# Performance work log

Hardware: AMD Instinct MI355X
Metric: run time of the kernel (lower is better)

The kernel has to match this reference:

```python
import math
import jax, jax.numpy as jnp
import numpy as np

N_TOKENS = 16384
IN_FEATURES = 4096
N_EXPERTS = 64
TOP_K = 2
CAPACITY_FACTOR = 1.25
# get_capacity(n_tokens * top_k, n_experts, capacity_factor)
CAPACITY = math.ceil(N_TOKENS * TOP_K / N_EXPERTS * CAPACITY_FACTOR)  # 640


def setup_inputs() -> dict:
    key = jax.random.key(0)
    kx, kw = jax.random.split(key)
    x = jax.random.normal(kx, (N_TOKENS, IN_FEATURES), dtype=jnp.float32)
    W = jax.random.normal(kw, (N_EXPERTS, IN_FEATURES), dtype=jnp.float32) * (1.0 / math.sqrt(IN_FEATURES))
    return {"x": x, "W": W}


def reference(x, W):
    # gate: Linear(in_features, n_experts, bias=False)
    logits = jnp.einsum("nd,ed->ne", x, W)  # [N, E]
    n, e = logits.shape

    # pre_softmax=False path: topk over logits then softmax over the k scores
    scores, top_idx = jax.lax.top_k(logits, TOP_K)              # [N, K]
    probs = jax.nn.softmax(scores.astype(jnp.float32), axis=-1).astype(logits.dtype)

    rows = jnp.arange(n)[:, None]                               # [N, 1]
    # scatter probs / ones into dense [N, E] masks (topk indices per row are unique)
    top_k_masked_gates = jnp.zeros_like(logits).at[rows, top_idx].set(probs)
    top_k_mask = jnp.zeros_like(logits).at[rows, top_idx].set(1.0)

    # capacity top-k along the token dim (dim=0) -> per-expert token selection
    _, cap_idx = jax.lax.top_k(top_k_masked_gates.T, CAPACITY)  # [E, CAP] token ids
    cap_mask = jnp.zeros_like(logits).at[cap_idx, jnp.arange(e)[:, None]].set(1.0)

    # pad_to_capacity=False branch
    final_mask = jnp.logical_and(top_k_mask > 0, cap_mask > 0)  # [N, E]
    drop_mask = jnp.logical_not(final_mask)
    exceed_mask = jnp.take_along_axis(drop_mask, top_idx, axis=1)  # [N, K]
    final_probs = probs * jnp.logical_not(exceed_mask)
    final_indices = jnp.where(exceed_mask, jnp.iinfo(jnp.int32).max, top_idx)
    tokens_per_expert_before_capacity = top_k_mask.sum(0)       # [E]

    return final_probs, final_indices, tokens_per_expert_before_capacity
```

## Files before the change

kernel.cpp:

```cpp
#include <hip/hip_runtime.h>
#include <math.h>

#define N_TOK  16384
#define DIM    4096
#define NE     64
#define CAP    640
#define KC     32
#define TM     128
#define NTILES (N_TOK / TM)


__global__ __launch_bounds__(256) void gemm_logits_kernel(
    const float* __restrict__ x, const float* __restrict__ W,
    float* __restrict__ partials, int ks) {
  const int tile  = blockIdx.x % NTILES;
  const int split = blockIdx.x / NTILES;
  const int klen  = DIM / ks;
  const int k0    = split * klen;
  const int t_base = tile * TM;

  __shared__ float xT[2][KC][TM + 4];
  __shared__ float wT[2][KC][NE + 4];

  const int tid = threadIdx.x;
  const int lr = tid >> 3;
  const int lc = tid & 7;
  const int tg = tid >> 3;
  const int eg = tid & 7;

  float acc[4][8];
#pragma unroll
  for (int i = 0; i < 4; ++i)
#pragma unroll
    for (int j = 0; j < 8; ++j) acc[i][j] = 0.f;

  float4 rx0, rx1, rx2, rx3, rw0, rw1;

  {
    const int kg = k0;
    rx0 = *(const float4*)(x + (size_t)(t_base + lr +  0) * DIM + kg + lc * 4);
    rx1 = *(const float4*)(x + (size_t)(t_base + lr + 32) * DIM + kg + lc * 4);
    rx2 = *(const float4*)(x + (size_t)(t_base + lr + 64) * DIM + kg + lc * 4);
    rx3 = *(const float4*)(x + (size_t)(t_base + lr + 96) * DIM + kg + lc * 4);
    rw0 = *(const float4*)(W + (size_t)(lr +  0) * DIM + kg + lc * 4);
    rw1 = *(const float4*)(W + (size_t)(lr + 32) * DIM + kg + lc * 4);
    xT[0][lc * 4 + 0][lr +  0] = rx0.x; xT[0][lc * 4 + 1][lr +  0] = rx0.y;
    xT[0][lc * 4 + 2][lr +  0] = rx0.z; xT[0][lc * 4 + 3][lr +  0] = rx0.w;
    xT[0][lc * 4 + 0][lr + 32] = rx1.x; xT[0][lc * 4 + 1][lr + 32] = rx1.y;
    xT[0][lc * 4 + 2][lr + 32] = rx1.z; xT[0][lc * 4 + 3][lr + 32] = rx1.w;
    xT[0][lc * 4 + 0][lr + 64] = rx2.x; xT[0][lc * 4 + 1][lr + 64] = rx2.y;
    xT[0][lc * 4 + 2][lr + 64] = rx2.z; xT[0][lc * 4 + 3][lr + 64] = rx2.w;
    xT[0][lc * 4 + 0][lr + 96] = rx3.x; xT[0][lc * 4 + 1][lr + 96] = rx3.y;
    xT[0][lc * 4 + 2][lr + 96] = rx3.z; xT[0][lc * 4 + 3][lr + 96] = rx3.w;
    wT[0][lc * 4 + 0][lr +  0] = rw0.x; wT[0][lc * 4 + 1][lr +  0] = rw0.y;
    wT[0][lc * 4 + 2][lr +  0] = rw0.z; wT[0][lc * 4 + 3][lr +  0] = rw0.w;
    wT[0][lc * 4 + 0][lr + 32] = rw1.x; wT[0][lc * 4 + 1][lr + 32] = rw1.y;
    wT[0][lc * 4 + 2][lr + 32] = rw1.z; wT[0][lc * 4 + 3][lr + 32] = rw1.w;
  }

  const int niter = klen / KC;
  for (int it = 0; it < niter; ++it) {
    const int cur = it & 1;
    const int nxt = cur ^ 1;
    const bool more = (it + 1 < niter);

    if (more) {
      const int kg = k0 + (it + 1) * KC;
      rx0 = *(const float4*)(x + (size_t)(t_base + lr +  0) * DIM + kg + lc * 4);
      rx1 = *(const float4*)(x + (size_t)(t_base + lr + 32) * DIM + kg + lc * 4);
      rx2 = *(const float4*)(x + (size_t)(t_base + lr + 64) * DIM + kg + lc * 4);
      rx3 = *(const float4*)(x + (size_t)(t_base + lr + 96) * DIM + kg + lc * 4);
      rw0 = *(const float4*)(W + (size_t)(lr +  0) * DIM + kg + lc * 4);
      rw1 = *(const float4*)(W + (size_t)(lr + 32) * DIM + kg + lc * 4);
    }

    __syncthreads();

#pragma unroll
    for (int k = 0; k < KC; ++k) {
      const float4 xv = *(const float4*)&xT[cur][k][tg * 4];
      const float4 w0 = *(const float4*)&wT[cur][k][eg * 8];
      const float4 w1 = *(const float4*)&wT[cur][k][eg * 8 + 4];
      const float xa[4] = {xv.x, xv.y, xv.z, xv.w};
      const float wa[8] = {w0.x, w0.y, w0.z, w0.w, w1.x, w1.y, w1.z, w1.w};
#pragma unroll
      for (int i = 0; i < 4; ++i)
#pragma unroll
        for (int j = 0; j < 8; ++j)
          acc[i][j] = fmaf(xa[i], wa[j], acc[i][j]);
    }

    if (more) {
      xT[nxt][lc * 4 + 0][lr +  0] = rx0.x; xT[nxt][lc * 4 + 1][lr +  0] = rx0.y;
      xT[nxt][lc * 4 + 2][lr +  0] = rx0.z; xT[nxt][lc * 4 + 3][lr +  0] = rx0.w;
      xT[nxt][lc * 4 + 0][lr + 32] = rx1.x; xT[nxt][lc * 4 + 1][lr + 32] = rx1.y;
      xT[nxt][lc * 4 + 2][lr + 32] = rx1.z; xT[nxt][lc * 4 + 3][lr + 32] = rx1.w;
      xT[nxt][lc * 4 + 0][lr + 64] = rx2.x; xT[nxt][lc * 4 + 1][lr + 64] = rx2.y;
      xT[nxt][lc * 4 + 2][lr + 64] = rx2.z; xT[nxt][lc * 4 + 3][lr + 64] = rx2.w;
      xT[nxt][lc * 4 + 0][lr + 96] = rx3.x; xT[nxt][lc * 4 + 1][lr + 96] = rx3.y;
      xT[nxt][lc * 4 + 2][lr + 96] = rx3.z; xT[nxt][lc * 4 + 3][lr + 96] = rx3.w;
      wT[nxt][lc * 4 + 0][lr +  0] = rw0.x; wT[nxt][lc * 4 + 1][lr +  0] = rw0.y;
      wT[nxt][lc * 4 + 2][lr +  0] = rw0.z; wT[nxt][lc * 4 + 3][lr +  0] = rw0.w;
      wT[nxt][lc * 4 + 0][lr + 32] = rw1.x; wT[nxt][lc * 4 + 1][lr + 32] = rw1.y;
      wT[nxt][lc * 4 + 2][lr + 32] = rw1.z; wT[nxt][lc * 4 + 3][lr + 32] = rw1.w;
    }
  }

  float* outp = partials + (size_t)split * N_TOK * NE;
#pragma unroll
  for (int i = 0; i < 4; ++i) {
    const int t = t_base + tg * 4 + i;
    const float4 v0 = make_float4(acc[i][0], acc[i][1], acc[i][2], acc[i][3]);
    const float4 v1 = make_float4(acc[i][4], acc[i][5], acc[i][6], acc[i][7]);
    *(float4*)(outp + (size_t)t * NE + eg * 8)     = v0;
    *(float4*)(outp + (size_t)t * NE + eg * 8 + 4) = v1;
  }
}

__global__ __launch_bounds__(256) void route_kernel(
    const float* __restrict__ partials, int ks,
    float* __restrict__ out, int* __restrict__ ws_idx,
    float* __restrict__ ws_probs, int* __restrict__ counts) {
  __shared__ int cnt[NE];
  const int tid = threadIdx.x;
  if (tid < NE) cnt[tid] = 0;
  __syncthreads();
  const int t = blockIdx.x * 256 + tid;

  float b1 = -INFINITY, b2 = -INFINITY;
  int i1 = 0, i2 = 0;
  for (int e = 0; e < NE; e += 4) {
    float4 s = *(const float4*)(partials + (size_t)t * NE + e);
    for (int sp = 1; sp < ks; ++sp) {
      const float4 v = *(const float4*)(partials + (size_t)sp * N_TOK * NE + (size_t)t * NE + e);
      s.x += v.x; s.y += v.y; s.z += v.z; s.w += v.w;
    }
    const float vv[4] = {s.x, s.y, s.z, s.w};
#pragma unroll
    for (int j = 0; j < 4; ++j) {
      const float v = vv[j];
      const int idx = e + j;
      if (v > b1)      { b2 = b1; i2 = i1; b1 = v; i1 = idx; }
      else if (v > b2) { b2 = v; i2 = idx; }
    }
  }
  const float ed = expf(b2 - b1);
  const float p1 = 1.0f / (1.0f + ed);
  const float p2 = ed / (1.0f + ed);

  out[(size_t)t * 2]     = p1;
  out[(size_t)t * 2 + 1] = p2;
  out[(size_t)N_TOK * 2 + t * 2]     = (float)i1;
  out[(size_t)N_TOK * 2 + t * 2 + 1] = (float)i2;
  ws_idx[t * 2] = i1;  ws_idx[t * 2 + 1] = i2;
  ws_probs[t * 2] = p1; ws_probs[t * 2 + 1] = p2;

  atomicAdd(&cnt[i1], 1);
  atomicAdd(&cnt[i2], 1);
  __syncthreads();
  if (tid < NE) atomicAdd(&counts[tid], cnt[tid]);
}

__global__ __launch_bounds__(256) void capacity_kernel(
    const int* __restrict__ counts, const int* __restrict__ ws_idx,
    const float* __restrict__ ws_probs, float* __restrict__ out) {
  const int e = blockIdx.x;
  const int cnt = counts[e];
  if (threadIdx.x == 0) out[(size_t)N_TOK * 4 + e] = (float)cnt;
  if (cnt <= CAP) return;
  for (int i = threadIdx.x; i < N_TOK * 2; i += 256) {
    if (ws_idx[i] != e) continue;
    const float p = ws_probs[i];
    const int tok = i >> 1;
    int rank = 0;
    for (int j = 0; j < N_TOK * 2; ++j) {
      if (ws_idx[j] != e) continue;
      const float q = ws_probs[j];
      if (q > p || (q == p && (j >> 1) < tok)) ++rank;
    }
    if (rank >= CAP) {
      out[i] = 0.0f;
      out[(size_t)N_TOK * 2 + i] = 2147483648.0f;
    }
  }
}

extern "C" void kernel_launch(void* const* d_in, const int* in_sizes, int n_in,
                              void* d_out, int out_size, void* d_ws, size_t ws_size,
                              hipStream_t stream) {
  const float* x = (const float*)d_in[0];
  const float* W = (const float*)d_in[1];
  float* out = (float*)d_out;

  char* ws = (char*)d_ws;
  int*   counts   = (int*)ws;
  int*   ws_idx   = (int*)(ws + 256);
  float* ws_probs = (float*)(ws + 256 + (size_t)N_TOK * 2 * 4);
  float* partials = (float*)(ws + 262400);

  const size_t base = 262400;
  const size_t per  = (size_t)N_TOK * NE * 4;
  int ks = 1;
  if (ws_size >= base + 8 * per)      ks = 8;
  else if (ws_size >= base + 4 * per) ks = 4;
  else if (ws_size >= base + 2 * per) ks = 2;

  hipMemsetAsync(counts, 0, NE * sizeof(int), stream);
  gemm_logits_kernel<<<NTILES * ks, 256, 0, stream>>>(x, W, partials, ks);
  route_kernel<<<N_TOK / 256, 256, 0, stream>>>(partials, ks, out, ws_idx, ws_probs, counts);
  capacity_kernel<<<NE, 256, 0, stream>>>(counts, ws_idx, ws_probs, out);
}
```

Before: 471.5 us.

## Load GEMM tiles directly into LDS with XOR-swizzled layout; restructure routing

The logits GEMM now fills LDS with global_load_lds straight from global memory, skipping the register staging and transposed scalar LDS stores. It uses an XOR-swizzled k-major layout so the float4 LDS reads avoid bank conflicts. The inner loop reads contiguous k-vectors per token and expert, and launch bounds now request 3 blocks per CU. The route kernel switches to 64-thread blocks and loads all partials up front for more memory-level parallelism. In exchange, register pressure rises and a single barrier per iteration must also cover the asynchronous LDS writes.

```diff
diff --git a/kernel.cpp b/kernel.cpp
--- a/kernel.cpp
+++ b/kernel.cpp
@@ -10,7 +10,12 @@
 #define NTILES (N_TOK / TM)
 
 
-__global__ __launch_bounds__(256) void gemm_logits_kernel(
+__device__ __forceinline__ void gl_lds16(const float* g, float* l) {
+  __builtin_amdgcn_global_load_lds((const __attribute__((address_space(1))) void*)g,
+                                   (__attribute__((address_space(3))) void*)l, 16, 0, 0);
+}
+
+__global__ __launch_bounds__(256, 3) void gemm_logits_kernel(
     const float* __restrict__ x, const float* __restrict__ W,
     float* __restrict__ partials, int ks) {
   const int tile  = blockIdx.x % NTILES;
@@ -19,14 +24,23 @@
   const int k0    = split * klen;
   const int t_base = tile * TM;
 
-  __shared__ float xT[2][KC][TM + 4];
-  __shared__ float wT[2][KC][NE + 4];
+  __shared__ float xs[2][KC * TM];
+  __shared__ float wss[2][KC * NE];
 
   const int tid = threadIdx.x;
-  const int lr = tid >> 3;
-  const int lc = tid & 7;
-  const int tg = tid >> 3;
-  const int eg = tid & 7;
+  const int tg  = tid >> 3;
+  const int eg  = tid & 7;
+  const int lk  = tid & 7;
+
+  const int klx  = 4 * (lk ^ ((tg >> 2) & 7));
+  const int klw0 = 4 * (lk ^ (tg >> 3));
+  const int klw1 = 4 * (lk ^ ((tg >> 3) + 4));
+
+  const float* xg  = x + (size_t)(t_base + tg) * DIM + k0 + klx;
+  const float* wg0 = W + (size_t)tg * DIM + k0 + klw0;
+  const float* wg1 = W + (size_t)(tg + 32) * DIM + k0 + klw1;
+  float* xl = &xs[0][0]  + tid * 4;
+  float* wl = &wss[0][0] + tid * 4;
 
   float acc[4][8];
 #pragma unroll
@@ -34,76 +48,63 @@
 #pragma unroll
     for (int j = 0; j < 8; ++j) acc[i][j] = 0.f;
 
-  float4 rx0, rx1, rx2, rx3, rw0, rw1;
+  const int niter = klen / KC;
 
   {
-    const int kg = k0;
-    rx0 = *(const float4*)(x + (size_t)(t_base + lr +  0) * DIM + kg + lc * 4);
-    rx1 = *(const float4*)(x + (size_t)(t_base + lr + 32) * DIM + kg + lc * 4);
-    rx2 = *(const float4*)(x + (size_t)(t_base + lr + 64) * DIM + kg + lc * 4);
-    rx3 = *(const float4*)(x + (size_t)(t_base + lr + 96) * DIM + kg + lc * 4);
-    rw0 = *(const float4*)(W + (size_t)(lr +  0) * DIM + kg + lc * 4);
-    rw1 = *(const float4*)(W + (size_t)(lr + 32) * DIM + kg + lc * 4);
-    xT[0][lc * 4 + 0][lr +  0] = rx0.x; xT[0][lc * 4 + 1][lr +  0] = rx0.y;
-    xT[0][lc * 4 + 2][lr +  0] = rx0.z; xT[0][lc * 4 + 3][lr +  0] = rx0.w;
-    xT[0][lc * 4 + 0][lr + 32] = rx1.x; xT[0][lc * 4 + 1][lr + 32] = rx1.y;
-    xT[0][lc * 4 + 2][lr + 32] = rx1.z; xT[0][lc * 4 + 3][lr + 32] = rx1.w;
-    xT[0][lc * 4 + 0][lr + 64] = rx2.x; xT[0][lc * 4 + 1][lr + 64] = rx2.y;
-    xT[0][lc * 4 + 2][lr + 64] = rx2.z; xT[0][lc * 4 + 3][lr + 64] = rx2.w;
-    xT[0][lc * 4 + 0][lr + 96] = rx3.x; xT[0][lc * 4 + 1][lr + 96] = rx3.y;
-    xT[0][lc * 4 + 2][lr + 96] = rx3.z; xT[0][lc * 4 + 3][lr + 96] = rx3.w;
-    wT[0][lc * 4 + 0][lr +  0] = rw0.x; wT[0][lc * 4 + 1][lr +  0] = rw0.y;
-    wT[0][lc * 4 + 2][lr +  0] = rw0.z; wT[0][lc * 4 + 3][lr +  0] = rw0.w;
-    wT[0][lc * 4 + 0][lr + 32] = rw1.x; wT[0][lc * 4 + 1][lr + 32] = rw1.y;
-    wT[0][lc * 4 + 2][lr + 32] = rw1.z; wT[0][lc * 4 + 3][lr + 32] = rw1.w;
-  }
-
-  const int niter = klen / KC;
+    gl_lds16(xg,            xl);
+    gl_lds16(xg + 32 * DIM, xl + 1024);
+    gl_lds16(xg + 64 * DIM, xl + 2048);
+    gl_lds16(xg + 96 * DIM, xl + 3072);
+    gl_lds16(wg0, wl);
+    gl_lds16(wg1, wl + 1024);
+  }
+  __syncthreads();
+
+  const int twz = tg & 7;
   for (int it = 0; it < niter; ++it) {
     const int cur = it & 1;
     const int nxt = cur ^ 1;
-    const bool more = (it + 1 < niter);
-
-    if (more) {
-      const int kg = k0 + (it + 1) * KC;
-      rx0 = *(const float4*)(x + (size_t)(t_base + lr +  0) * DIM + kg + lc * 4);
-      rx1 = *(const float4*)(x + (size_t)(t_base + lr + 32) * DIM + kg + lc * 4);
-      rx2 = *(const float4*)(x + (size_t)(t_base + lr + 64) * DIM + kg + lc * 4);
-      rx3 = *(const float4*)(x + (size_t)(t_base + lr + 96) * DIM + kg + lc * 4);
-      rw0 = *(const float4*)(W + (size_t)(lr +  0) * DIM + kg + lc * 4);
-      rw1 = *(const float4*)(W + (size_t)(lr + 32) * DIM + kg + lc * 4);
+
+    if (it + 1 < niter) {
+      const int ko = (it + 1) * KC;
+      gl_lds16(xg + ko,            xl + nxt * 4096);
+      gl_lds16(xg + ko + 32 * DIM, xl + nxt * 4096 + 1024);
+      gl_lds16(xg + ko + 64 * DIM, xl + nxt * 4096 + 2048);
+      gl_lds16(xg + ko + 96 * DIM, xl + nxt * 4096 + 3072);
+      gl_lds16(wg0 + ko, wl + nxt * 2048);
+      gl_lds16(wg1 + ko, wl + nxt * 2048 + 1024);
+    }
+
+    const float* xb = &xs[cur][0];
+    const float* wb = &wss[cur][0];
+#pragma unroll
+    for (int kq = 0; kq < 8; ++kq) {
+      const int xo = 4 * (kq ^ twz);
+      const int wo = 4 * (kq ^ eg);
+      float xa[16];
+#pragma unroll
+      for (int i = 0; i < 4; ++i) {
+        const float4 v = *(const float4*)(xb + (4 * tg + i) * 32 + xo);
+        xa[i * 4 + 0] = v.x; xa[i * 4 + 1] = v.y; xa[i * 4 + 2] = v.z; xa[i * 4 + 3] = v.w;
+      }
+      float wa[32];
+#pragma unroll
+      for (int j = 0; j < 8; ++j) {
+        const float4 v = *(const float4*)(wb + (8 * eg + j) * 32 + wo);
+        wa[j * 4 + 0] = v.x; wa[j * 4 + 1] = v.y; wa[j * 4 + 2] = v.z; wa[j * 4 + 3] = v.w;
+      }
+#pragma unroll
+      for (int i = 0; i < 4; ++i)
+#pragma unroll
+        for (int j = 0; j < 8; ++j) {
+          acc[i][j] = fmaf(xa[i * 4 + 0], wa[j * 4 + 0], acc[i][j]);
+          acc[i][j] = fmaf(xa[i * 4 + 1], wa[j * 4 + 1], acc[i][j]);
+          acc[i][j] = fmaf(xa[i * 4 + 2], wa[j * 4 + 2], acc[i][j]);
+          acc[i][j] = fmaf(xa[i * 4 + 3], wa[j * 4 + 3], acc[i][j]);
+        }
     }
 
     __syncthreads();
-
-#pragma unroll
-    for (int k = 0; k < KC; ++k) {
-      const float4 xv = *(const float4*)&xT[cur][k][tg * 4];
-      const float4 w0 = *(const float4*)&wT[cur][k][eg * 8];
-      const float4 w1 = *(const float4*)&wT[cur][k][eg * 8 + 4];
-      const float xa[4] = {xv.x, xv.y, xv.z, xv.w};
-      const float wa[8] = {w0.x, w0.y, w0.z, w0.w, w1.x, w1.y, w1.z, w1.w};
-#pragma unroll
-      for (int i = 0; i < 4; ++i)
-#pragma unroll
-        for (int j = 0; j < 8; ++j)
-          acc[i][j] = fmaf(xa[i], wa[j], acc[i][j]);
-    }
-
-    if (more) {
-      xT[nxt][lc * 4 + 0][lr +  0] = rx0.x; xT[nxt][lc * 4 + 1][lr +  0] = rx0.y;
-      xT[nxt][lc * 4 + 2][lr +  0] = rx0.z; xT[nxt][lc * 4 + 3][lr +  0] = rx0.w;
-      xT[nxt][lc * 4 + 0][lr + 32] = rx1.x; xT[nxt][lc * 4 + 1][lr + 32] = rx1.y;
-      xT[nxt][lc * 4 + 2][lr + 32] = rx1.z; xT[nxt][lc * 4 + 3][lr + 32] = rx1.w;
-      xT[nxt][lc * 4 + 0][lr + 64] = rx2.x; xT[nxt][lc * 4 + 1][lr + 64] = rx2.y;
-      xT[nxt][lc * 4 + 2][lr + 64] = rx2.z; xT[nxt][lc * 4 + 3][lr + 64] = rx2.w;
-      xT[nxt][lc * 4 + 0][lr + 96] = rx3.x; xT[nxt][lc * 4 + 1][lr + 96] = rx3.y;
-      xT[nxt][lc * 4 + 2][lr + 96] = rx3.z; xT[nxt][lc * 4 + 3][lr + 96] = rx3.w;
-      wT[nxt][lc * 4 + 0][lr +  0] = rw0.x; wT[nxt][lc * 4 + 1][lr +  0] = rw0.y;
-      wT[nxt][lc * 4 + 2][lr +  0] = rw0.z; wT[nxt][lc * 4 + 3][lr +  0] = rw0.w;
-      wT[nxt][lc * 4 + 0][lr + 32] = rw1.x; wT[nxt][lc * 4 + 1][lr + 32] = rw1.y;
-      wT[nxt][lc * 4 + 2][lr + 32] = rw1.z; wT[nxt][lc * 4 + 3][lr + 32] = rw1.w;
-    }
   }
 
   float* outp = partials + (size_t)split * N_TOK * NE;
@@ -117,29 +118,40 @@
   }
 }
 
-__global__ __launch_bounds__(256) void route_kernel(
+__global__ __launch_bounds__(64) void route_kernel(
     const float* __restrict__ partials, int ks,
     float* __restrict__ out, int* __restrict__ ws_idx,
     float* __restrict__ ws_probs, int* __restrict__ counts) {
   __shared__ int cnt[NE];
   const int tid = threadIdx.x;
-  if (tid < NE) cnt[tid] = 0;
+  cnt[tid] = 0;
   __syncthreads();
-  const int t = blockIdx.x * 256 + tid;
+  const int t = blockIdx.x * 64 + tid;
+
+  float4 s[16];
+  {
+    const float* p = partials + (size_t)t * NE;
+#pragma unroll
+    for (int c = 0; c < 16; ++c) s[c] = *(const float4*)(p + 4 * c);
+  }
+  for (int sp = 1; sp < ks; ++sp) {
+    const float* p = partials + (size_t)sp * N_TOK * NE + (size_t)t * NE;
+#pragma unroll
+    for (int c = 0; c < 16; ++c) {
+      const float4 v = *(const float4*)(p + 4 * c);
+      s[c].x += v.x; s[c].y += v.y; s[c].z += v.z; s[c].w += v.w;
+    }
+  }
 
   float b1 = -INFINITY, b2 = -INFINITY;
   int i1 = 0, i2 = 0;
-  for (int e = 0; e < NE; e += 4) {
-    float4 s = *(const float4*)(partials + (size_t)t * NE + e);
-    for (int sp = 1; sp < ks; ++sp) {
-      const float4 v = *(const float4*)(partials + (size_t)sp * N_TOK * NE + (size_t)t * NE + e);
-      s.x += v.x; s.y += v.y; s.z += v.z; s.w += v.w;
-    }
-    const float vv[4] = {s.x, s.y, s.z, s.w};
+#pragma unroll
+  for (int c = 0; c < 16; ++c) {
+    const float vv[4] = {s[c].x, s[c].y, s[c].z, s[c].w};
 #pragma unroll
     for (int j = 0; j < 4; ++j) {
       const float v = vv[j];
-      const int idx = e + j;
+      const int idx = c * 4 + j;
       if (v > b1)      { b2 = b1; i2 = i1; b1 = v; i1 = idx; }
       else if (v > b2) { b2 = v; i2 = idx; }
     }
@@ -158,7 +170,7 @@
   atomicAdd(&cnt[i1], 1);
   atomicAdd(&cnt[i2], 1);
   __syncthreads();
-  if (tid < NE) atomicAdd(&counts[tid], cnt[tid]);
+  atomicAdd(&counts[tid], cnt[tid]);
 }
 
 __global__ __launch_bounds__(256) void capacity_kernel(
@@ -207,6 +219,6 @@
 
   hipMemsetAsync(counts, 0, NE * sizeof(int), stream);
   gemm_logits_kernel<<<NTILES * ks, 256, 0, stream>>>(x, W, partials, ks);
-  route_kernel<<<N_TOK / 256, 256, 0, stream>>>(partials, ks, out, ws_idx, ws_probs, counts);
+  route_kernel<<<N_TOK / 64, 64, 0, stream>>>(partials, ks, out, ws_idx, ws_probs, counts);
   capacity_kernel<<<NE, 256, 0, stream>>>(counts, ws_idx, ws_probs, out);
 }
```

New measurement: 443.1 us. -6.0%, faster.
